# Optimization experiments

Hardware: AMD Instinct MI355X
Metric: run time of the kernel (lower is better)

Reference implementation:

```python
import jax, jax.numpy as jnp
import numpy as np

N, D_IM, D_CLI = 2048, 1024, 64
EPS = 1e-12  # F.normalize eps


def setup_inputs() -> dict:
    key = jax.random.key(0)
    k1, k2, k3, k4 = jax.random.split(key, 4)
    phi_im = jax.random.normal(k1, (N, D_IM), dtype=jnp.float32)
    phi_cli = jax.random.normal(k2, (N, D_CLI), dtype=jnp.float32)
    t = jax.random.randint(k3, (N, 2), 0, 3, dtype=jnp.int64)
    traumatic = jax.random.randint(k4, (N,), 0, 2, dtype=jnp.int64)
    return {"phi_im": phi_im, "phi_cli": phi_cli, "t": t, "traumatic": traumatic}


def _l2norm(x):
    n = jnp.sqrt(jnp.sum(x * x, axis=1, keepdims=True))
    return x / jnp.maximum(n, EPS)


def _pair_block(S, ma, mb):
    # S: [N,N] full cosine similarity; ma, mb: [N] bool group masks.
    valid = ma[:, None] & mb[None, :]
    mat = jnp.where(valid, S, 0.0)            # scatter-into-zero matrix semantics
    masked = jnp.where(valid, S, jnp.inf)     # masked argmin = nearest (least similar) pair
    flat = jnp.argmin(masked.reshape(-1))
    i = flat // S.shape[1]
    j = flat % S.shape[1]
    return mat, masked.reshape(-1)[flat], jnp.stack([i, j])


def reference(phi_im, phi_cli, t, traumatic):
    im_n = _l2norm(phi_im)
    cli_n = _l2norm(phi_cli)
    # single batched GEMM replaces the per-pair python loops
    S_im = im_n @ im_n.T    # [N,N]
    S_cli = cli_n @ cli_n.T  # [N,N]

    t1 = t[:, 1]
    m0 = (t1 == 0) & (traumatic == 1)
    m1 = t1 == 1
    m2 = t1 == 2

    mats, vals, idxs = [], [], []
    for S in (S_im, S_cli):
        for (ma, mb) in ((m0, m1), (m0, m2), (m1, m2)):
            mat, v, ij = _pair_block(S, ma, mb)
            mats.append(mat)
            vals.append(v)
            idxs.append(ij)
    sims = jnp.stack(mats)           # [6, N, N]: im_01, im_02, im_12, cli_01, cli_02, cli_12
    min_vals = jnp.stack(vals)       # [6]
    min_idx = jnp.stack(idxs)        # [6, 2]
    return sims, min_vals, min_idx
```

## Files before the change

### kernel.cpp

```cpp
#include <hip/hip_runtime.h>
#include <stdint.h>

#define NROW 2048
#define D_IM 1024
#define D_CLI 64
#define EPSF 1e-12f
#define NN ((size_t)NROW * (size_t)NROW)
#define GRID_GEMM 800

typedef __attribute__((ext_vector_type(8))) short bf16x8;
typedef __attribute__((ext_vector_type(4))) float f32x4;

#define OFF_PACKED   0
#define OFF_CNT      64
#define OFF_CAT      128
#define OFF_LISTS    8320
#define OFF_POS      32896
#define OFF_COLINFO  41216
#define OFF_INVIM    65792
#define OFF_INVCLI   73984
#define OFF_PIM      82176
#define OFF_PCLI     8470784
#define OFF_SC       8995072

__device__ __forceinline__ unsigned int enc_f32(float x) {
    unsigned int u = __float_as_uint(x);
    return (u & 0x80000000u) ? ~u : (u | 0x80000000u);
}
__device__ __forceinline__ unsigned short bf16rn(float x) {
    unsigned int u = __float_as_uint(x);
    return (unsigned short)((u + 0x7FFFu + ((u >> 16) & 1u)) >> 16);
}
__device__ __forceinline__ float bf16tof(unsigned short h) {
    return __uint_as_float(((unsigned int)h) << 16);
}

__global__ __launch_bounds__(256)
void prepscan_kernel(const float* __restrict__ phi_im,
                     const float* __restrict__ phi_cli,
                     const int* __restrict__ t,
                     const int* __restrict__ traumatic,
                     float* __restrict__ inv_im,
                     float* __restrict__ inv_cli,
                     char* __restrict__ pim,
                     char* __restrict__ pcli,
                     int* __restrict__ cnt,
                     int* __restrict__ catArr,
                     int* __restrict__ lists,
                     int* __restrict__ posIn,
                     unsigned int* __restrict__ colinfo,
                     unsigned long long* __restrict__ packed,
                     float* __restrict__ out) {
    __shared__ unsigned long long shmem[256];
    const int tid = threadIdx.x;

    if (blockIdx.x > NROW) {
        const int row = blockIdx.x - (NROW + 1);
        const int t1 = t[2 * row + 1];
        const int tr = traumatic[row];
        if (t1 == 0 && tr == 1) return;
        float* orow = out + (size_t)row * NROW;
        const f32x4 z4 = (f32x4){0.f, 0.f, 0.f, 0.f};
        __builtin_nontemporal_store(z4, (f32x4*)orow + tid);
        __builtin_nontemporal_store(z4, (f32x4*)orow + tid + 256);
        return;
    }

    if (blockIdx.x == NROW) {
        int cats[8];
        unsigned long long mycnt = 0;
        #pragma unroll
        for (int e = 0; e < 8; e++) {
            int r = tid * 8 + e;
            int t1 = t[2 * r + 1];
            int tr = traumatic[r];
            int c = (t1 == 1) ? 1 : ((t1 == 2) ? 2 : ((tr == 1) ? 0 : 3));
            cats[e] = c;
            catArr[r] = c;
            if (c < 3) mycnt += 1ULL << (21 * c);
        }
        shmem[tid] = mycnt;
        __syncthreads();
        for (int off = 1; off < 256; off <<= 1) {
            unsigned long long v = (tid >= off) ? shmem[tid - off] : 0ULL;
            __syncthreads();
            shmem[tid] += v;
            __syncthreads();
        }
        unsigned long long excl = shmem[tid] - mycnt;
        unsigned long long tot = shmem[255];
        unsigned int loc[3];
        #pragma unroll
        for (int c = 0; c < 3; c++)
            loc[c] = (unsigned int)(excl >> (21 * c)) & 0x1FFFFFu;
        #pragma unroll
        for (int e = 0; e < 8; e++) {
            int r = tid * 8 + e;
            int c = cats[e];
            unsigned int slot = 0xFFFFFFFFu;
            if (c < 3) {
                slot = loc[c]++;
                lists[c * 2048 + slot] = r;
                posIn[r] = (int)slot;
            }
            colinfo[0 * 2048 + r] = (c == 1) ? slot : 0xFFFFFFFFu;
            colinfo[1 * 2048 + r] = (c == 2) ? slot : 0xFFFFFFFFu;
            colinfo[2 * 2048 + r] = (c == 2) ? slot : 0xFFFFFFFFu;
        }
        if (tid == 0) {
            cnt[0] = (int)(tot & 0x1FFFFFu);
            cnt[1] = (int)((tot >> 21) & 0x1FFFFFu);
            cnt[2] = (int)((tot >> 42) & 0x1FFFFFu);
            cnt[3] = 0;
        }
        if (tid < 6) packed[tid] = 0xFFFFFFFFFFFFFFFFULL;
        return;
    }

    float* sred = (float*)shmem;
    const int r = blockIdx.x;

    float4 v = ((const float4*)(phi_im + (size_t)r * D_IM))[tid];
    float a[4] = {v.x, v.y, v.z, v.w};
    unsigned short h4[4], l4[4];
    #pragma unroll
    for (int e = 0; e < 4; e++) {
        h4[e] = bf16rn(a[e]);
        l4[e] = bf16rn(a[e] - bf16tof(h4[e]));
    }
    {
        char* rowb = pim + (size_t)r * 4096 + (tid >> 1) * 32 + (tid & 1) * 8;
        *(ushort4*)rowb = make_ushort4(h4[0], h4[1], h4[2], h4[3]);
        *(ushort4*)(rowb + 16) = make_ushort4(l4[0], l4[1], l4[2], l4[3]);
    }
    sred[tid] = a[0] * a[0] + a[1] * a[1] + a[2] * a[2] + a[3] * a[3];
    __syncthreads();
    for (int off = 128; off > 0; off >>= 1) {
        if (tid < off) sred[tid] += sred[tid + off];
        __syncthreads();
    }
    if (tid == 0) inv_im[r] = 1.0f / fmaxf(sqrtf(sred[0]), EPSF);

    if (tid < 16) {
        float4 c = ((const float4*)(phi_cli + (size_t)r * D_CLI))[tid];
        float b[4] = {c.x, c.y, c.z, c.w};
        unsigned short ch[4], cl[4];
        #pragma unroll
        for (int e = 0; e < 4; e++) {
            ch[e] = bf16rn(b[e]);
            cl[e] = bf16rn(b[e] - bf16tof(ch[e]));
        }
        char* rowb = pcli + (size_t)r * 256 + (tid >> 1) * 32 + (tid & 1) * 8;
        *(ushort4*)rowb = make_ushort4(ch[0], ch[1], ch[2], ch[3]);
        *(ushort4*)(rowb + 16) = make_ushort4(cl[0], cl[1], cl[2], cl[3]);
    }
    if (tid < 64) {
        float c = phi_cli[(size_t)r * D_CLI + tid];
        float cs = c * c;
        #pragma unroll
        for (int off = 32; off > 0; off >>= 1) cs += __shfl_down(cs, off, 64);
        if (tid == 0) inv_cli[r] = 1.0f / fmaxf(sqrtf(cs), EPSF);
    }
}

#define LOAD_SET(s, AH, AL, BH, BL)                                        \
    {                                                                      \
        const int kb_ = (s) * 128;                                         \
        _Pragma("unroll") for (int mt = 0; mt < 4; mt++) {                 \
            AH[mt] = *(const bf16x8*)(pX + offA[mt] + kb_);                \
            AL[mt] = *(const bf16x8*)(pX + offA[mt] + kb_ + 16);           \
            BH[mt] = *(const bf16x8*)(pX + offB[mt] + kb_);                \
            BL[mt] = *(const bf16x8*)(pX + offB[mt] + kb_ + 16);           \
        }                                                                  \
    }
#define MFMA_SET(AH, AL, BH, BL)                                           \
    _Pragma("unroll") for (int mt = 0; mt < 4; mt++)                       \
        _Pragma("unroll") for (int nt = 0; nt < 4; nt++) {                 \
            acc[mt][nt] = __builtin_amdgcn_mfma_f32_16x16x32_bf16(         \
                AH[mt], BH[nt], acc[mt][nt], 0, 0, 0);                     \
            acc[mt][nt] = __builtin_amdgcn_mfma_f32_16x16x32_bf16(         \
                AH[mt], BL[nt], acc[mt][nt], 0, 0, 0);                     \
            acc[mt][nt] = __builtin_amdgcn_mfma_f32_16x16x32_bf16(         \
                AL[mt], BH[nt], acc[mt][nt], 0, 0, 0);                     \
        }

__global__ __launch_bounds__(256, 2)
void gemm_kernel(const char* __restrict__ pim,
                 const char* __restrict__ pcli,
                 const float* __restrict__ inv_im,
                 const float* __restrict__ inv_cli,
                 const int* __restrict__ cnt,
                 const int* __restrict__ lists,
                 const int* __restrict__ catArr,
                 unsigned short* __restrict__ Sc,
                 float* __restrict__ out,
                 unsigned long long* __restrict__ packed) {
    const int tid = threadIdx.x;

    if (blockIdx.x >= GRID_GEMM) {
        const int b = blockIdx.x - GRID_GEMM;
        const int pzf = 1 + (b >> 11);
        const int row = b & 2047;
        const int p = (pzf < 3) ? pzf : pzf - 3;
        const int rowcat = (p == 2) ? 1 : 0;
        if (catArr[row] == rowcat) return;
        float* orow = out + (size_t)pzf * NN + (size_t)row * NROW;
        const f32x4 z4 = (f32x4){0.f, 0.f, 0.f, 0.f};
        __builtin_nontemporal_store(z4, (f32x4*)orow + tid);
        __builtin_nontemporal_store(z4, (f32x4*)orow + tid + 256);
        return;
    }

    __shared__ float sIA[64], sIB[64];
    __shared__ int sRA[64], sRB[64];
    __shared__ f32x4 sAcc[4][4][3][64];

    const int n0 = cnt[0], n1 = cnt[1], n2 = cnt[2];
    const int tA = (n0 + 63) >> 6, tB = (n1 + 63) >> 6, tC = (n2 + 63) >> 6;
    const int T0 = tA * tB, T1 = tA * tC, T2 = tB * tC;
    const int tot = T0 + T1 + T2;
    int bid = blockIdx.x;
    if (bid >= 2 * tot) return;
    int z = 0;
    if (bid >= tot) { z = 1; bid -= tot; }
    const size_t s0 = (size_t)(tA << 6) * (tB << 6);
    const size_t s1 = (size_t)(tA << 6) * (tC << 6);
    const size_t s2 = (size_t)(tB << 6) * (tC << 6);
    size_t scoff = z ? (s0 + s1 + s2) : 0;
    int gx, nA, nB, nBpad, pp;
    const int *lA, *lB;
    if (bid < T0)           { pp = 0; gx = tB; nA = n0; nB = n1; lA = lists;        lB = lists + 2048; nBpad = tB << 6; }
    else if (bid < T0 + T1) { bid -= T0;      scoff += s0;      pp = 1; gx = tC; nA = n0; nB = n2; lA = lists;        lB = lists + 4096; nBpad = tC << 6; }
    else                    { bid -= T0 + T1; scoff += s0 + s1; pp = 2; gx = tC; nA = n1; nB = n2; lA = lists + 2048; lB = lists + 4096; nBpad = tC << 6; }
    const int by = bid / gx, bx = bid % gx;
    const int i0 = by << 6, j0 = bx << 6;
    const int pz = z * 3 + pp;

    const char* __restrict__ pX = z ? pcli : pim;
    const float* __restrict__ inv = z ? inv_cli : inv_im;
    const int steps = z ? (D_CLI / 32) : (D_IM / 32);
    const size_t stride = z ? 256 : 4096;
    const int lane = tid & 63;
    const int wid = tid >> 6;

    if (tid < 64) {
        int ia = lA[min(i0 + tid, nA - 1)];
        int ib = lB[min(j0 + tid, nB - 1)];
        sRA[tid] = ia; sRB[tid] = ib;
        sIA[tid] = inv[ia]; sIB[tid] = inv[ib];
    }
    __syncthreads();

    const int mrow = lane & 15;
    const int quad = lane >> 4;
    size_t offA[4], offB[4];
    #pragma unroll
    for (int mt = 0; mt < 4; mt++) {
        offA[mt] = (size_t)sRA[mt * 16 + mrow] * stride + quad * 32;
        offB[mt] = (size_t)sRB[mt * 16 + mrow] * stride + quad * 32;
    }

    f32x4 acc[4][4];
    #pragma unroll
    for (int mt = 0; mt < 4; mt++)
        #pragma unroll
        for (int nt = 0; nt < 4; nt++)
            acc[mt][nt] = (f32x4){0.f, 0.f, 0.f, 0.f};

    const int spw = (steps + 3) >> 2;
    const int sBeg = wid * spw;
    const int sEnd = min(steps, sBeg + spw);

    bf16x8 A0h[4], A0l[4], B0h[4], B0l[4];
    bf16x8 A1h[4], A1l[4], B1h[4], B1l[4];
    if (sBeg < sEnd) {
        LOAD_SET(sBeg, A0h, A0l, B0h, B0l);
        for (int s = sBeg; s < sEnd; s += 2) {
            if (s + 1 < sEnd) LOAD_SET(s + 1, A1h, A1l, B1h, B1l);
            MFMA_SET(A0h, A0l, B0h, B0l);
            if (s + 2 < sEnd) LOAD_SET(s + 2, A0h, A0l, B0h, B0l);
            if (s + 1 < sEnd) MFMA_SET(A1h, A1l, B1h, B1l);
        }
    }

    #pragma unroll
    for (int mt = 0; mt < 4; mt++)
        #pragma unroll
        for (int nt = 0; nt < 4; nt++)
            if (nt != wid) sAcc[wid][mt][nt - (nt > wid ? 1 : 0)][lane] = acc[mt][nt];
    __syncthreads();

    unsigned long long best = 0xFFFFFFFFFFFFFFFFULL;
    const int cloc = wid * 16 + mrow;
    const float ivb = sIB[cloc];
    const unsigned int jcol = (unsigned int)sRB[cloc];
    #pragma unroll
    for (int mt = 0; mt < 4; mt++) {
        f32x4 facc = acc[mt][wid];
        #pragma unroll
        for (int w2 = 0; w2 < 4; w2++)
            if (w2 != wid) facc += sAcc[w2][mt][wid - (wid > w2 ? 1 : 0)][lane];
        #pragma unroll
        for (int rr = 0; rr < 4; rr++) {
            const int rloc = mt * 16 + quad * 4 + rr;
            float sv = facc[rr] * (sIA[rloc] * ivb);
            Sc[scoff + (size_t)(i0 + rloc) * nBpad + (j0 + cloc)] = bf16rn(sv);
            unsigned long long pk =
                ((unsigned long long)enc_f32(sv) << 32) |
                ((unsigned int)sRA[rloc] * (unsigned int)NROW + jcol);
            if (pk < best) best = pk;
        }
    }
    #pragma unroll
    for (int off = 32; off > 0; off >>= 1) {
        unsigned long long o = __shfl_down(best, off, 64);
        if (o < best) best = o;
    }
    if (lane == 0) atomicMin(&packed[pz], best);
}

__global__ __launch_bounds__(256)
void writer_kernel(const unsigned short* __restrict__ Sc,
                   const int* __restrict__ cnt,
                   const int* __restrict__ catArr,
                   const int* __restrict__ posIn,
                   const unsigned int* __restrict__ colinfo,
                   float* __restrict__ out,
                   const unsigned long long* __restrict__ packed) {
    const int b = blockIdx.x;
    const int tid = threadIdx.x;
    if (b == 6 * NROW) {
        const int p = tid;
        if (p < 6) {
            unsigned long long pk = packed[p];
            float v;
            unsigned int flat;
            if (pk == 0xFFFFFFFFFFFFFFFFULL) { v = __builtin_huge_valf(); flat = 0u; }
            else {
                unsigned int key = (unsigned int)(pk >> 32);
                flat = (unsigned int)pk;
                unsigned int bits = (key & 0x80000000u) ? (key ^ 0x80000000u) : ~key;
                v = __uint_as_float(bits);
            }
            out[6 * NN + p] = v;
            out[6 * NN + 6 + 2 * p + 0] = (float)(flat >> 11);
            out[6 * NN + 6 + 2 * p + 1] = (float)(flat & 2047u);
        }
        return;
    }
    const int pz = b >> 11;
    const int row = b & 2047;
    const int z = pz / 3, p = pz - 3 * z;

    const int rowcat = (p == 2) ? 1 : 0;
    if (catArr[row] != rowcat) {
        if (pz < 4) return;
        float* orow = out + (size_t)pz * NN + (size_t)row * NROW;
        const f32x4 z4 = (f32x4){0.f, 0.f, 0.f, 0.f};
        __builtin_nontemporal_store(z4, (f32x4*)orow + tid);
        __builtin_nontemporal_store(z4, (f32x4*)orow + tid + 256);
        return;
    }

    float* orow = out + (size_t)pz * NN + (size_t)row * NROW;

    const int n0 = cnt[0], n1 = cnt[1], n2 = cnt[2];
    const int tA = (n0 + 63) >> 6, tB = (n1 + 63) >> 6, tC = (n2 + 63) >> 6;
    const size_t s0 = (size_t)(tA << 6) * (tB << 6);
    const size_t s1 = (size_t)(tA << 6) * (tC << 6);
    const size_t s2 = (size_t)(tB << 6) * (tC << 6);
    size_t scoff = z ? (s0 + s1 + s2) : 0;
    int nBpad;
    if (p == 0)      { nBpad = tB << 6; }
    else if (p == 1) { scoff += s0;      nBpad = tC << 6; }
    else             { scoff += s0 + s1; nBpad = tC << 6; }

    const unsigned short* srow = Sc + scoff + (size_t)posIn[row] * nBpad;
    const uint4* cinfo4 = (const uint4*)(colinfo + p * 2048);

    #pragma unroll
    for (int seg = 0; seg < 2; seg++) {
        const int j4 = tid + seg * 256;
        uint4 inf = cinfo4[j4];
        f32x4 vv;
        vv[0] = (inf.x != 0xFFFFFFFFu) ? bf16tof(srow[inf.x]) : 0.f;
        vv[1] = (inf.y != 0xFFFFFFFFu) ? bf16tof(srow[inf.y]) : 0.f;
        vv[2] = (inf.z != 0xFFFFFFFFu) ? bf16tof(srow[inf.z]) : 0.f;
        vv[3] = (inf.w != 0xFFFFFFFFu) ? bf16tof(srow[inf.w]) : 0.f;
        __builtin_nontemporal_store(vv, (f32x4*)orow + j4);
    }
}

extern "C" void kernel_launch(void* const* d_in, const int* in_sizes, int n_in,
                              void* d_out, int out_size, void* d_ws, size_t ws_size,
                              hipStream_t stream) {
    const float* phi_im = (const float*)d_in[0];
    const float* phi_cli = (const float*)d_in[1];
    const int* t = (const int*)d_in[2];
    const int* traumatic = (const int*)d_in[3];
    float* out = (float*)d_out;

    char* ws = (char*)d_ws;
    unsigned long long* packed = (unsigned long long*)(ws + OFF_PACKED);
    int* cnt = (int*)(ws + OFF_CNT);
    int* catArr = (int*)(ws + OFF_CAT);
    int* lists = (int*)(ws + OFF_LISTS);
    int* posIn = (int*)(ws + OFF_POS);
    unsigned int* colinfo = (unsigned int*)(ws + OFF_COLINFO);
    float* inv_im = (float*)(ws + OFF_INVIM);
    float* inv_cli = (float*)(ws + OFF_INVCLI);
    char* pim = ws + OFF_PIM;
    char* pcli = ws + OFF_PCLI;
    unsigned short* Sc = (unsigned short*)(ws + OFF_SC);

    prepscan_kernel<<<2 * NROW + 1, 256, 0, stream>>>(
        phi_im, phi_cli, t, traumatic, inv_im, inv_cli, pim, pcli,
        cnt, catArr, lists, posIn, colinfo, packed, out);
    gemm_kernel<<<GRID_GEMM + 3 * NROW, 256, 0, stream>>>(
        pim, pcli, inv_im, inv_cli, cnt, lists, catArr, Sc, out, packed);
    writer_kernel<<<6 * NROW + 1, 256, 0, stream>>>(Sc, cnt, catArr, posIn,
                                                    colinfo, out, packed);
}
```

Baseline: 179.3 us.

## Switch GEMM from split-K across waves to 2x2 output-tile wave decomposition

Each of the four waves previously computed the full 64x64 tile over a quarter of K, then reduced partial accumulators through a large shared-memory buffer with a barrier. Now each wave owns a 32x32 quadrant of the output over the full K range, which removes the shared-memory reduction, the barrier and most accumulator registers. The trade-off is lower operand reuse per wave (each A/B fragment is loaded by two waves) and a longer serial K loop per wave, which matters for the short 64-dim clinical GEMM.

```diff
diff --git a/kernel.cpp b/kernel.cpp
--- a/kernel.cpp
+++ b/kernel.cpp
@@ -166,22 +166,22 @@
 #define LOAD_SET(s, AH, AL, BH, BL)                                        \
     {                                                                      \
         const int kb_ = (s) * 128;                                         \
-        _Pragma("unroll") for (int mt = 0; mt < 4; mt++) {                 \
-            AH[mt] = *(const bf16x8*)(pX + offA[mt] + kb_);                \
-            AL[mt] = *(const bf16x8*)(pX + offA[mt] + kb_ + 16);           \
-            BH[mt] = *(const bf16x8*)(pX + offB[mt] + kb_);                \
-            BL[mt] = *(const bf16x8*)(pX + offB[mt] + kb_ + 16);           \
+        _Pragma("unroll") for (int q = 0; q < 2; q++) {                    \
+            AH[q] = *(const bf16x8*)(pX + offA[q] + kb_);                  \
+            AL[q] = *(const bf16x8*)(pX + offA[q] + kb_ + 16);             \
+            BH[q] = *(const bf16x8*)(pX + offB[q] + kb_);                  \
+            BL[q] = *(const bf16x8*)(pX + offB[q] + kb_ + 16);             \
         }                                                                  \
     }
 #define MFMA_SET(AH, AL, BH, BL)                                           \
-    _Pragma("unroll") for (int mt = 0; mt < 4; mt++)                       \
-        _Pragma("unroll") for (int nt = 0; nt < 4; nt++) {                 \
-            acc[mt][nt] = __builtin_amdgcn_mfma_f32_16x16x32_bf16(         \
-                AH[mt], BH[nt], acc[mt][nt], 0, 0, 0);                     \
-            acc[mt][nt] = __builtin_amdgcn_mfma_f32_16x16x32_bf16(         \
-                AH[mt], BL[nt], acc[mt][nt], 0, 0, 0);                     \
-            acc[mt][nt] = __builtin_amdgcn_mfma_f32_16x16x32_bf16(         \
-                AL[mt], BH[nt], acc[mt][nt], 0, 0, 0);                     \
+    _Pragma("unroll") for (int lm = 0; lm < 2; lm++)                       \
+        _Pragma("unroll") for (int ln = 0; ln < 2; ln++) {                 \
+            acc[lm][ln] = __builtin_amdgcn_mfma_f32_16x16x32_bf16(         \
+                AH[lm], BH[ln], acc[lm][ln], 0, 0, 0);                     \
+            acc[lm][ln] = __builtin_amdgcn_mfma_f32_16x16x32_bf16(         \
+                AH[lm], BL[ln], acc[lm][ln], 0, 0, 0);                     \
+            acc[lm][ln] = __builtin_amdgcn_mfma_f32_16x16x32_bf16(         \
+                AL[lm], BH[ln], acc[lm][ln], 0, 0, 0);                     \
         }
 
 __global__ __launch_bounds__(256, 2)
@@ -213,7 +213,6 @@
 
     __shared__ float sIA[64], sIB[64];
     __shared__ int sRA[64], sRB[64];
-    __shared__ f32x4 sAcc[4][4][3][64];
 
     const int n0 = cnt[0], n1 = cnt[1], n2 = cnt[2];
     const int tA = (n0 + 63) >> 6, tB = (n1 + 63) >> 6, tC = (n2 + 63) >> 6;
@@ -242,6 +241,8 @@
     const size_t stride = z ? 256 : 4096;
     const int lane = tid & 63;
     const int wid = tid >> 6;
+    const int wr = wid >> 1;
+    const int wc = wid & 1;
 
     if (tid < 64) {
         int ia = lA[min(i0 + tid, nA - 1)];
@@ -253,64 +254,49 @@
 
     const int mrow = lane & 15;
     const int quad = lane >> 4;
-    size_t offA[4], offB[4];
-    #pragma unroll
-    for (int mt = 0; mt < 4; mt++) {
-        offA[mt] = (size_t)sRA[mt * 16 + mrow] * stride + quad * 32;
-        offB[mt] = (size_t)sRB[mt * 16 + mrow] * stride + quad * 32;
-    }
-
-    f32x4 acc[4][4];
-    #pragma unroll
-    for (int mt = 0; mt < 4; mt++)
-        #pragma unroll
-        for (int nt = 0; nt < 4; nt++)
-            acc[mt][nt] = (f32x4){0.f, 0.f, 0.f, 0.f};
-
-    const int spw = (steps + 3) >> 2;
-    const int sBeg = wid * spw;
-    const int sEnd = min(steps, sBeg + spw);
-
-    bf16x8 A0h[4], A0l[4], B0h[4], B0l[4];
-    bf16x8 A1h[4], A1l[4], B1h[4], B1l[4];
-    if (sBeg < sEnd) {
-        LOAD_SET(sBeg, A0h, A0l, B0h, B0l);
-        for (int s = sBeg; s < sEnd; s += 2) {
-            if (s + 1 < sEnd) LOAD_SET(s + 1, A1h, A1l, B1h, B1l);
-            MFMA_SET(A0h, A0l, B0h, B0l);
-            if (s + 2 < sEnd) LOAD_SET(s + 2, A0h, A0l, B0h, B0l);
-            if (s + 1 < sEnd) MFMA_SET(A1h, A1l, B1h, B1l);
-        }
-    }
-
-    #pragma unroll
-    for (int mt = 0; mt < 4; mt++)
-        #pragma unroll
-        for (int nt = 0; nt < 4; nt++)
-            if (nt != wid) sAcc[wid][mt][nt - (nt > wid ? 1 : 0)][lane] = acc[mt][nt];
-    __syncthreads();
+    size_t offA[2], offB[2];
+    #pragma unroll
+    for (int q = 0; q < 2; q++) {
+        offA[q] = (size_t)sRA[(wr * 2 + q) * 16 + mrow] * stride + quad * 32;
+        offB[q] = (size_t)sRB[(wc * 2 + q) * 16 + mrow] * stride + quad * 32;
+    }
+
+    f32x4 acc[2][2];
+    #pragma unroll
+    for (int lm = 0; lm < 2; lm++)
+        #pragma unroll
+        for (int ln = 0; ln < 2; ln++)
+            acc[lm][ln] = (f32x4){0.f, 0.f, 0.f, 0.f};
+
+    bf16x8 A0h[2], A0l[2], B0h[2], B0l[2];
+    bf16x8 A1h[2], A1l[2], B1h[2], B1l[2];
+    LOAD_SET(0, A0h, A0l, B0h, B0l);
+    for (int s = 0; s < steps; s += 2) {
+        if (s + 1 < steps) LOAD_SET(s + 1, A1h, A1l, B1h, B1l);
+        MFMA_SET(A0h, A0l, B0h, B0l);
+        if (s + 2 < steps) LOAD_SET(s + 2, A0h, A0l, B0h, B0l);
+        if (s + 1 < steps) MFMA_SET(A1h, A1l, B1h, B1l);
+    }
 
     unsigned long long best = 0xFFFFFFFFFFFFFFFFULL;
-    const int cloc = wid * 16 + mrow;
-    const float ivb = sIB[cloc];
-    const unsigned int jcol = (unsigned int)sRB[cloc];
-    #pragma unroll
-    for (int mt = 0; mt < 4; mt++) {
-        f32x4 facc = acc[mt][wid];
-        #pragma unroll
-        for (int w2 = 0; w2 < 4; w2++)
-            if (w2 != wid) facc += sAcc[w2][mt][wid - (wid > w2 ? 1 : 0)][lane];
-        #pragma unroll
-        for (int rr = 0; rr < 4; rr++) {
-            const int rloc = mt * 16 + quad * 4 + rr;
-            float sv = facc[rr] * (sIA[rloc] * ivb);
-            Sc[scoff + (size_t)(i0 + rloc) * nBpad + (j0 + cloc)] = bf16rn(sv);
-            unsigned long long pk =
-                ((unsigned long long)enc_f32(sv) << 32) |
-                ((unsigned int)sRA[rloc] * (unsigned int)NROW + jcol);
-            if (pk < best) best = pk;
-        }
-    }
+    #pragma unroll
+    for (int lm = 0; lm < 2; lm++)
+        #pragma unroll
+        for (int ln = 0; ln < 2; ln++) {
+            const int cloc = (wc * 2 + ln) * 16 + mrow;
+            const float ivb = sIB[cloc];
+            const unsigned int jcol = (unsigned int)sRB[cloc];
+            #pragma unroll
+            for (int rr = 0; rr < 4; rr++) {
+                const int rloc = (wr * 2 + lm) * 16 + quad * 4 + rr;
+                float sv = acc[lm][ln][rr] * (sIA[rloc] * ivb);
+                Sc[scoff + (size_t)(i0 + rloc) * nBpad + (j0 + cloc)] = bf16rn(sv);
+                unsigned long long pk =
+                    ((unsigned long long)enc_f32(sv) << 32) |
+                    ((unsigned int)sRA[rloc] * (unsigned int)NROW + jcol);
+                if (pk < best) best = pk;
+            }
+        }
     #pragma unroll
     for (int off = 32; off > 0; off >>= 1) {
         unsigned long long o = __shfl_down(best, off, 64);
```

Result: slower. 190.3 us (+6.2%).
